# Optimization experiments

Measured on AMD Instinct MI355X. Metric: run time of the kernel, lower is better.

## Reference

```python
import math
import jax, jax.numpy as jnp
import numpy as np

DIM_IN = 2048
DIM_OUT = 2048
BLOCK = 128
N_BLOCKS = 256
SPARSITY = 0.1
BATCH = 8192


def setup_inputs() -> dict:
    key = jax.random.key(0)
    k1, k2, k3, k4, k5 = jax.random.split(key, 5)
    x = jax.random.normal(k1, (BATCH, DIM_IN), dtype=jnp.float32)
    weight = jax.random.normal(k2, (DIM_IN, DIM_OUT), dtype=jnp.float32) * (1.0 / math.sqrt(DIM_IN))
    bias = jax.random.normal(k3, (DIM_OUT,), dtype=jnp.float32) * 0.01
    gate_w = jax.random.normal(k4, (DIM_IN, N_BLOCKS), dtype=jnp.float32) * (1.0 / math.sqrt(DIM_IN))
    gate_b = jax.random.normal(k5, (N_BLOCKS,), dtype=jnp.float32) * 0.01
    return {"x": x, "weight": weight, "bias": bias, "gate_w": gate_w, "gate_b": gate_b}


def _sparsify1d(g):
    # k-th largest kept per row; threshold, mask, renormalize (Sparsify1D)
    n = g.shape[-1]
    k = int(math.ceil(SPARSITY * n))
    topval = jax.lax.top_k(g, k)[0][:, -1:]          # (B, 1) k-th largest value
    res = jnp.where(g >= topval, g, jnp.zeros_like(g))
    return res / (jnp.sum(res, axis=-1, keepdims=True) / n)


def reference(x, weight, bias, gate_w, gate_b):
    B = x.shape[0]
    s = DIM_IN // BLOCK                               # 16 block-rows/cols
    # gate network: Linear -> Sparsify1D
    g = _sparsify1d(x @ gate_w + gate_b)              # (B, s*s)
    gb = g.reshape(B, s, s)                           # (B, s_in, s_out)
    xb = x.reshape(B, s, BLOCK)                       # (B, s_in, block)
    Wb = weight.reshape(s, BLOCK, s, BLOCK)           # (s_in, block, s_out, block)
    # gated block matrix-vector multiply:
    # y[b,q,n] = sum_{p,m} g[b,p,q] * x[b,p,m] * W[p,m,q,n]
    y = jnp.einsum('bpq,bpm,pmqn->bqn', gb, xb, Wb)
    return y.reshape(B, DIM_OUT) + bias
```

## Files before the change

kernel.cpp:

```cpp
#include <hip/hip_runtime.h>
#include <hip/hip_bf16.h>
#include <stdint.h>

#define BATCH  8192
#define DIN    2048
#define DOUT   2048
#define NB     256
#define KSEL   26

typedef __attribute__((ext_vector_type(4))) float f32x4;
typedef __attribute__((ext_vector_type(8))) __bf16 bf16x8;
typedef __attribute__((ext_vector_type(8))) unsigned short u16x8;
typedef __attribute__((ext_vector_type(4))) unsigned short u16x4;

__device__ __forceinline__ float bf2f(unsigned short u){
  union { unsigned int i; float f; } v; v.i = ((unsigned int)u) << 16; return v.f;
}
__device__ __forceinline__ unsigned short f2bf(float f){
  union { float f; unsigned int i; } v; v.f = f;
  unsigned int x = v.i;
  return (unsigned short)((x + 0x7FFFu + ((x >> 16) & 1u)) >> 16);
}

__global__ void conv_x(const float* __restrict__ x, unsigned short* __restrict__ xb, int n4)
{
  const int stride = gridDim.x * blockDim.x;
  for (int i = blockIdx.x * blockDim.x + threadIdx.x; i < n4; i += stride){
    f32x4 v = ((const f32x4*)x)[i];
    u16x4 o;
    #pragma unroll
    for (int j = 0; j < 4; j++) o[j] = f2bf(v[j]);
    ((u16x4*)xb)[i] = o;
  }
}

__global__ __launch_bounds__(256) void conv_wt(const float* __restrict__ w, unsigned short* __restrict__ wt)
{
  __shared__ float tl[64][65];
  const int k0 = blockIdx.x * 64;
  const int n0 = blockIdx.y * 64;
  const int c  = threadIdx.x & 63;
  const int r4 = threadIdx.x >> 6;
  #pragma unroll
  for (int i = 0; i < 16; i++){
    const int r = r4 * 16 + i;
    tl[r][c] = w[(size_t)(k0 + r) * DOUT + n0 + c];
  }
  __syncthreads();
  #pragma unroll
  for (int i = 0; i < 16; i++){
    const int n = r4 * 16 + i;
    wt[(size_t)(n0 + n) * DIN + k0 + c] = f2bf(tl[c][n]);
  }
}

__global__ __launch_bounds__(256) void gate_gemm(
    const float* __restrict__ x, const float* __restrict__ gw,
    float* __restrict__ part)
{
  __shared__ float xT[64][68];
  __shared__ float wT[64][260];
  const int b0 = blockIdx.x * 64;
  const int ks = blockIdx.y;
  const int t  = threadIdx.x;
  const int ct = t & 31;
  const int rt = t >> 5;

  float acc[8][2][4];
  #pragma unroll
  for (int i = 0; i < 8; i++)
    #pragma unroll
    for (int h = 0; h < 2; h++)
      #pragma unroll
      for (int j = 0; j < 4; j++) acc[i][h][j] = 0.f;

  const int koff = ks * 1024;
  for (int kc = 0; kc < 1024; kc += 64){
    {
      const int row = t & 63, kb = (t >> 6) * 16;
      const float* src = &x[(size_t)(b0 + row) * DIN + koff + kc + kb];
      #pragma unroll
      for (int q4 = 0; q4 < 4; q4++){
        f32x4 a = *(const f32x4*)(src + q4 * 4);
        #pragma unroll
        for (int j = 0; j < 4; j++) xT[kb + q4 * 4 + j][row] = a[j];
      }
    }
    {
      const int c4 = (t & 63) * 4, kq = t >> 6;
      #pragma unroll
      for (int i = 0; i < 16; i++){
        const int k = kq * 16 + i;
        *(f32x4*)&wT[k][c4] = *(const f32x4*)&gw[(size_t)(koff + kc + k) * NB + c4];
      }
    }
    __syncthreads();
    #pragma unroll 8
    for (int k = 0; k < 64; k++){
      f32x4 xv0 = *(const f32x4*)&xT[k][rt * 8];
      f32x4 xv1 = *(const f32x4*)&xT[k][rt * 8 + 4];
      f32x4 wv0 = *(const f32x4*)&wT[k][ct * 4];
      f32x4 wv1 = *(const f32x4*)&wT[k][ct * 4 + 128];
      #pragma unroll
      for (int j = 0; j < 4; j++){
        #pragma unroll
        for (int i = 0; i < 4; i++){
          acc[i][0][j]     = fmaf(xv0[i], wv0[j], acc[i][0][j]);
          acc[i + 4][0][j] = fmaf(xv1[i], wv0[j], acc[i + 4][0][j]);
          acc[i][1][j]     = fmaf(xv0[i], wv1[j], acc[i][1][j]);
          acc[i + 4][1][j] = fmaf(xv1[i], wv1[j], acc[i + 4][1][j]);
        }
      }
    }
    __syncthreads();
  }
  float* dst = part + (size_t)ks * BATCH * NB;
  #pragma unroll
  for (int i = 0; i < 8; i++){
    const int row = b0 + rt * 8 + i;
    #pragma unroll
    for (int h = 0; h < 2; h++){
      f32x4 o;
      #pragma unroll
      for (int j = 0; j < 4; j++) o[j] = acc[i][h][j];
      *(f32x4*)&dst[(size_t)row * NB + ct * 4 + h * 128] = o;
    }
  }
}

__global__ __launch_bounds__(256) void topk(float* __restrict__ part, const float* __restrict__ gb)
{
  const int lane = threadIdx.x & 63;
  const int row  = blockIdx.x * 4 + (threadIdx.x >> 6);
  f32x4* p0 = (f32x4*)&part[(size_t)row * NB];
  const f32x4* p1 = (const f32x4*)&part[(size_t)(BATCH + row) * NB];
  const f32x4* gbv = (const f32x4*)gb;
  f32x4 v = p0[lane] + p1[lane] + gbv[lane];

  const float NEG = -3.402823466e38f;
  float w0 = v[0], w1 = v[1], w2 = v[2], w3 = v[3];
  float thr = 0.f;
  for (int it = 0; it < KSEL; it++){
    float lm = fmaxf(fmaxf(w0, w1), fmaxf(w2, w3));
    float wm = lm;
    #pragma unroll
    for (int off = 32; off; off >>= 1) wm = fmaxf(wm, __shfl_xor(wm, off, 64));
    unsigned long long ball = __ballot(lm == wm);
    int first = __ffsll(ball) - 1;
    if (lane == first){
      if      (w0 == wm) w0 = NEG;
      else if (w1 == wm) w1 = NEG;
      else if (w2 == wm) w2 = NEG;
      else               w3 = NEG;
    }
    thr = wm;
  }
  float s = 0.f;
  #pragma unroll
  for (int j = 0; j < 4; j++) s += (v[j] >= thr) ? v[j] : 0.f;
  #pragma unroll
  for (int off = 32; off; off >>= 1) s += __shfl_xor(s, off, 64);
  const float d = s * (1.0f / NB);
  f32x4 o;
  #pragma unroll
  for (int j = 0; j < 4; j++) o[j] = (v[j] >= thr) ? v[j] / d : 0.f;
  p0[lane] = o;
}

__global__ __launch_bounds__(256) void main_gemm(
    const unsigned short* __restrict__ xb,
    const unsigned short* __restrict__ wt,
    const float* __restrict__ g,
    const float* __restrict__ bias,
    float* __restrict__ out)
{
  __shared__ unsigned short xa[128][72];
  __shared__ unsigned short wb[128][72];
  __shared__ float gl[128 * 17];

  const int q    = blockIdx.x;
  const int b0   = blockIdx.y * 128;
  const int t    = threadIdx.x;
  const int lane = t & 63;
  const int wid  = t >> 6;
  const int wr   = (wid >> 1) * 64;
  const int wc   = (wid & 1) * 64;
  const int l15  = lane & 15;
  const int l4   = lane >> 4;

  for (int e = t; e < 128 * 16; e += 256){
    const int r = e >> 4, p = e & 15;
    gl[r * 17 + p] = g[(size_t)(b0 + r) * NB + p * 16 + q];
  }

  f32x4 acc[4][4];
  #pragma unroll
  for (int m = 0; m < 4; m++)
    #pragma unroll
    for (int n = 0; n < 4; n++) acc[m][n] = (f32x4)0.0f;

  const int row_s = t >> 1;
  const int half  = t & 1;

  for (int kp = 0; kp < 32; kp++){
    const int p = kp >> 1;
    __syncthreads();
    {
      const float gate = gl[row_s * 17 + p];
      const unsigned short* src = &xb[(size_t)(b0 + row_s) * DIN + kp * 64 + half * 32];
      unsigned short* dst = &xa[row_s][half * 32];
      #pragma unroll
      for (int c = 0; c < 4; c++){
        u16x8 u = *(const u16x8*)(src + c * 8);
        u16x8 o;
        #pragma unroll
        for (int j = 0; j < 8; j++) o[j] = f2bf(bf2f(u[j]) * gate);
        *(u16x8*)(dst + c * 8) = o;
      }
    }
    {
      const unsigned short* src = &wt[(size_t)(q * 128 + row_s) * DIN + kp * 64 + half * 32];
      unsigned short* dst = &wb[row_s][half * 32];
      #pragma unroll
      for (int c = 0; c < 4; c++)
        *(u16x8*)(dst + c * 8) = *(const u16x8*)(src + c * 8);
    }
    __syncthreads();
    #pragma unroll
    for (int ksi = 0; ksi < 2; ksi++){
      const int kk = ksi * 32 + l4 * 8;
      bf16x8 a[4], b[4];
      #pragma unroll
      for (int m = 0; m < 4; m++)
        a[m] = *(const bf16x8*)&xa[wr + m * 16 + l15][kk];
      #pragma unroll
      for (int n = 0; n < 4; n++)
        b[n] = *(const bf16x8*)&wb[wc + n * 16 + l15][kk];
      #pragma unroll
      for (int m = 0; m < 4; m++)
        #pragma unroll
        for (int n = 0; n < 4; n++)
          acc[m][n] = __builtin_amdgcn_mfma_f32_16x16x32_bf16(a[m], b[n], acc[m][n], 0, 0, 0);
    }
  }

  #pragma unroll
  for (int n = 0; n < 4; n++){
    const int col = q * 128 + wc + n * 16 + l15;
    const float bv = bias[col];
    #pragma unroll
    for (int m = 0; m < 4; m++){
      #pragma unroll
      for (int r = 0; r < 4; r++){
        const int row = b0 + wr + m * 16 + l4 * 4 + r;
        out[(size_t)row * DOUT + col] = acc[m][n][r] + bv;
      }
    }
  }
}

extern "C" void kernel_launch(void* const* d_in, const int* in_sizes, int n_in,
                              void* d_out, int out_size, void* d_ws, size_t ws_size,
                              hipStream_t stream)
{
  const float* x    = (const float*)d_in[0];
  const float* w    = (const float*)d_in[1];
  const float* bias = (const float*)d_in[2];
  const float* gw   = (const float*)d_in[3];
  const float* gb   = (const float*)d_in[4];
  float* out = (float*)d_out;

  float*          part = (float*)d_ws;
  unsigned short* xb   = (unsigned short*)((char*)d_ws + (size_t)16 * 1024 * 1024);
  unsigned short* wtb  = (unsigned short*)((char*)d_ws + (size_t)48 * 1024 * 1024);

  conv_x   <<<2048, 256, 0, stream>>>(x, xb, BATCH * DIN / 4);
  conv_wt  <<<dim3(DIN / 64, DOUT / 64), 256, 0, stream>>>(w, wtb);
  gate_gemm<<<dim3(BATCH / 64, 2), 256, 0, stream>>>(x, gw, part);
  topk     <<<BATCH / 4, 256, 0, stream>>>(part, gb);
  main_gemm<<<dim3(16, BATCH / 128), 256, 0, stream>>>(xb, wtb, part, bias, out);
}
```

Before: 294.0 us.

## Fuse x bf16 conversion into gate GEMM and shrink gate tiles

Removes the separate conv_x kernel by having gate_gemm write the bf16 copy of x while it loads the x tile, which saves one full read of x and one launch. The gate GEMM tile is cut from 64 to 32 rows and 64 to 32 k-steps, so each thread now holds an 8-element accumulator block instead of a 16-element one and the grid doubles. The manual round-to-nearest bf16 conversion is replaced with the compiler's native cast, including in main_gemm. The smaller tiles lower per-thread arithmetic intensity and increase LDS traffic per FMA in the gate GEMM.

```diff
diff --git a/kernel.cpp b/kernel.cpp
--- a/kernel.cpp
+++ b/kernel.cpp
@@ -21,17 +21,9 @@
   unsigned int x = v.i;
   return (unsigned short)((x + 0x7FFFu + ((x >> 16) & 1u)) >> 16);
 }
-
-__global__ void conv_x(const float* __restrict__ x, unsigned short* __restrict__ xb, int n4)
-{
-  const int stride = gridDim.x * blockDim.x;
-  for (int i = blockIdx.x * blockDim.x + threadIdx.x; i < n4; i += stride){
-    f32x4 v = ((const f32x4*)x)[i];
-    u16x4 o;
-    #pragma unroll
-    for (int j = 0; j < 4; j++) o[j] = f2bf(v[j]);
-    ((u16x4*)xb)[i] = o;
-  }
+__device__ __forceinline__ unsigned short f2bf_c(float f){
+  __bf16 b = (__bf16)f;
+  union { __bf16 b; unsigned short u; } v; v.b = b; return v.u;
 }
 
 __global__ __launch_bounds__(256) void conv_wt(const float* __restrict__ w, unsigned short* __restrict__ wt)
@@ -56,75 +48,64 @@
 
 __global__ __launch_bounds__(256) void gate_gemm(
     const float* __restrict__ x, const float* __restrict__ gw,
-    float* __restrict__ part)
-{
-  __shared__ float xT[64][68];
-  __shared__ float wT[64][260];
-  const int b0 = blockIdx.x * 64;
+    float* __restrict__ part, unsigned short* __restrict__ xb)
+{
+  __shared__ float xT[32][36];
+  __shared__ float wT[32][260];
+  const int b0 = blockIdx.x * 32;
   const int ks = blockIdx.y;
   const int t  = threadIdx.x;
   const int ct = t & 31;
   const int rt = t >> 5;
 
-  float acc[8][2][4];
-  #pragma unroll
-  for (int i = 0; i < 8; i++)
-    #pragma unroll
-    for (int h = 0; h < 2; h++)
-      #pragma unroll
-      for (int j = 0; j < 4; j++) acc[i][h][j] = 0.f;
+  f32x4 acc0[4], acc1[4];
+  #pragma unroll
+  for (int i = 0; i < 4; i++){ acc0[i] = (f32x4)0.0f; acc1[i] = (f32x4)0.0f; }
+
+  const int sr  = t >> 3;
+  const int sk  = (t & 7) * 4;
+  const int wk  = (t >> 6) * 8;
+  const int wc4 = (t & 63) * 4;
 
   const int koff = ks * 1024;
-  for (int kc = 0; kc < 1024; kc += 64){
-    {
-      const int row = t & 63, kb = (t >> 6) * 16;
-      const float* src = &x[(size_t)(b0 + row) * DIN + koff + kc + kb];
-      #pragma unroll
-      for (int q4 = 0; q4 < 4; q4++){
-        f32x4 a = *(const f32x4*)(src + q4 * 4);
-        #pragma unroll
-        for (int j = 0; j < 4; j++) xT[kb + q4 * 4 + j][row] = a[j];
-      }
-    }
-    {
-      const int c4 = (t & 63) * 4, kq = t >> 6;
-      #pragma unroll
-      for (int i = 0; i < 16; i++){
-        const int k = kq * 16 + i;
-        *(f32x4*)&wT[k][c4] = *(const f32x4*)&gw[(size_t)(koff + kc + k) * NB + c4];
+  for (int kc = 0; kc < 1024; kc += 32){
+    {
+      const size_t gi = (size_t)(b0 + sr) * DIN + koff + kc + sk;
+      f32x4 a = *(const f32x4*)&x[gi];
+      u16x4 ob;
+      #pragma unroll
+      for (int j = 0; j < 4; j++) ob[j] = f2bf_c(a[j]);
+      *(u16x4*)&xb[gi] = ob;
+      #pragma unroll
+      for (int j = 0; j < 4; j++) xT[sk + j][sr] = a[j];
+    }
+    {
+      #pragma unroll
+      for (int i = 0; i < 8; i++){
+        const int k = wk + i;
+        *(f32x4*)&wT[k][wc4] = *(const f32x4*)&gw[(size_t)(koff + kc + k) * NB + wc4];
       }
     }
     __syncthreads();
     #pragma unroll 8
-    for (int k = 0; k < 64; k++){
-      f32x4 xv0 = *(const f32x4*)&xT[k][rt * 8];
-      f32x4 xv1 = *(const f32x4*)&xT[k][rt * 8 + 4];
+    for (int k = 0; k < 32; k++){
+      f32x4 xv  = *(const f32x4*)&xT[k][rt * 4];
       f32x4 wv0 = *(const f32x4*)&wT[k][ct * 4];
       f32x4 wv1 = *(const f32x4*)&wT[k][ct * 4 + 128];
       #pragma unroll
-      for (int j = 0; j < 4; j++){
-        #pragma unroll
-        for (int i = 0; i < 4; i++){
-          acc[i][0][j]     = fmaf(xv0[i], wv0[j], acc[i][0][j]);
-          acc[i + 4][0][j] = fmaf(xv1[i], wv0[j], acc[i + 4][0][j]);
-          acc[i][1][j]     = fmaf(xv0[i], wv1[j], acc[i][1][j]);
-          acc[i + 4][1][j] = fmaf(xv1[i], wv1[j], acc[i + 4][1][j]);
-        }
+      for (int i = 0; i < 4; i++){
+        acc0[i] += xv[i] * wv0;
+        acc1[i] += xv[i] * wv1;
       }
     }
     __syncthreads();
   }
   float* dst = part + (size_t)ks * BATCH * NB;
   #pragma unroll
-  for (int i = 0; i < 8; i++){
-    const int row = b0 + rt * 8 + i;
-    #pragma unroll
-    for (int h = 0; h < 2; h++){
-      f32x4 o;
-      #pragma unroll
-      for (int j = 0; j < 4; j++) o[j] = acc[i][h][j];
-      *(f32x4*)&dst[(size_t)row * NB + ct * 4 + h * 128] = o;
-    }
+  for (int i = 0; i < 4; i++){
+    const int row = b0 + rt * 4 + i;
+    *(f32x4*)&dst[(size_t)row * NB + ct * 4]       = acc0[i];
+    *(f32x4*)&dst[(size_t)row * NB + ct * 4 + 128] = acc1[i];
   }
 }
 
@@ -214,7 +195,7 @@
         u16x8 u = *(const u16x8*)(src + c * 8);
         u16x8 o;
         #pragma unroll
-        for (int j = 0; j < 8; j++) o[j] = f2bf(bf2f(u[j]) * gate);
+        for (int j = 0; j < 8; j++) o[j] = f2bf_c(bf2f(u[j]) * gate);
         *(u16x8*)(dst + c * 8) = o;
       }
     }
@@ -271,12 +252,11 @@
   float* out = (float*)d_out;
 
   float*          part = (float*)d_ws;
-  unsigned short* xb   = (unsigned short*)((char*)d_ws + (size_t)16 * 1024 * 1024);
-  unsigned short* wtb  = (unsigned short*)((char*)d_ws + (size_t)48 * 1024 * 1024);
-
-  conv_x   <<<2048, 256, 0, stream>>>(x, xb, BATCH * DIN / 4);
+  unsigned short* wtb  = (unsigned short*)((char*)d_ws + (size_t)16 * 1024 * 1024);
+  unsigned short* xbb  = (unsigned short*)((char*)d_ws + (size_t)24 * 1024 * 1024);
+
   conv_wt  <<<dim3(DIN / 64, DOUT / 64), 256, 0, stream>>>(w, wtb);
-  gate_gemm<<<dim3(BATCH / 64, 2), 256, 0, stream>>>(x, gw, part);
+  gate_gemm<<<dim3(BATCH / 32, 2), 256, 0, stream>>>(x, gw, part, xbb);
   topk     <<<BATCH / 4, 256, 0, stream>>>(part, gb);
-  main_gemm<<<dim3(16, BATCH / 128), 256, 0, stream>>>(xb, wtb, part, bias, out);
-}
+  main_gemm<<<dim3(16, BATCH / 128), 256, 0, stream>>>(xbb, wtb, part, bias, out);
+}
```

Result: faster. 269.2 us (-8.5%).
